# Optimization experiments

Hardware: AMD Instinct MI355X
Metric: run time of the kernel (lower is better)

## Reference

```python
import jax, jax.numpy as jnp
import numpy as np

DIM = 1280
NUM_HEADS = 16
HEAD_DIM = DIM // NUM_HEADS  # 80
SEQ = 3072


def rotate_half(x):
    half = x.shape[-1] // 2
    return jnp.concatenate([-x[..., half:], x[..., :half]], axis=-1)


def apply_rotary_pos_emb_vision(t, freqs):
    # t: [seq, heads, head_dim]; freqs: [seq, head_dim//2]
    emb = jnp.concatenate([freqs, freqs], axis=-1)  # [seq, head_dim]
    cos = jnp.cos(emb)[:, None, :]
    sin = jnp.sin(emb)[:, None, :]
    return t * cos + rotate_half(t) * sin


def setup_inputs() -> dict:
    key = jax.random.key(0)
    k1, k2, k3, k4, k5 = jax.random.split(key, 5)
    hidden_states = jax.random.normal(k1, (SEQ, DIM), dtype=jnp.float32)
    rotary_pos_emb = jax.random.uniform(k2, (SEQ, HEAD_DIM // 2), dtype=jnp.float32) * 10.0
    cu_seqlens = jnp.arange(5, dtype=jnp.int32) * (SEQ // 4)  # [0,768,1536,2304,3072]
    s = 1.0 / np.sqrt(DIM)
    qkv_w = jax.random.normal(k3, (3 * DIM, DIM), dtype=jnp.float32) * s
    qkv_b = jnp.zeros((3 * DIM,), dtype=jnp.float32)
    proj_w = jax.random.normal(k4, (DIM, DIM), dtype=jnp.float32) * s
    proj_b = jnp.zeros((DIM,), dtype=jnp.float32)
    return {
        "hidden_states": hidden_states,
        "rotary_pos_emb": rotary_pos_emb,
        "cu_seqlens": cu_seqlens,
        "qkv_w": qkv_w,
        "qkv_b": qkv_b,
        "proj_w": proj_w,
        "proj_b": proj_b,
    }


def reference(hidden_states, rotary_pos_emb, cu_seqlens, qkv_w, qkv_b, proj_w, proj_b):
    seq = hidden_states.shape[0]
    qkv = hidden_states @ qkv_w.T + qkv_b  # [seq, 3*dim]
    qkv = qkv.reshape(seq, 3, NUM_HEADS, HEAD_DIM)
    q, k, v = qkv[:, 0], qkv[:, 1], qkv[:, 2]  # each [seq, heads, head_dim]

    q = apply_rotary_pos_emb_vision(q, rotary_pos_emb)
    k = apply_rotary_pos_emb_vision(k, rotary_pos_emb)

    # block-diagonal mask from cu_seqlens: tokens attend only within own segment
    pos = jnp.arange(seq)
    seg = jnp.searchsorted(cu_seqlens[1:], pos, side="right")  # segment id per token
    mask = seg[:, None] == seg[None, :]  # [seq, seq] bool

    # [heads, seq, head_dim]
    qh = q.transpose(1, 0, 2)
    kh = k.transpose(1, 0, 2)
    vh = v.transpose(1, 0, 2)

    scale = 1.0 / np.sqrt(HEAD_DIM)
    scores = jnp.einsum("hqd,hkd->hqk", qh, kh) * scale
    scores = jnp.where(mask[None], scores, jnp.finfo(scores.dtype).min)
    attn = jax.nn.softmax(scores, axis=-1)
    out = jnp.einsum("hqk,hkd->hqd", attn, vh)  # [heads, seq, head_dim]

    out = out.transpose(1, 0, 2).reshape(seq, DIM)
    return out @ proj_w.T + proj_b
```

## Files before the change

kernel.cpp:

```cpp
#include <hip/hip_runtime.h>
#include <cstdint>
#include <cstddef>

#define SEQ 3072
#define DIM 1280
#define NH 16
#define HD 80

typedef __attribute__((ext_vector_type(8))) short s16x8;
typedef __attribute__((ext_vector_type(4))) float f32x4;
typedef unsigned short u16;
typedef unsigned int u32;
typedef unsigned long long u64;

__device__ __forceinline__ u16 f2bf(float f) {
  u32 u = __builtin_bit_cast(u32, f);
  u32 r = (u + 0x7FFFu + ((u >> 16) & 1u)) >> 16;
  return (u16)r;
}
__device__ __forceinline__ float bf2f(u16 b) {
  u32 u = ((u32)b) << 16;
  return __builtin_bit_cast(float, u);
}
__device__ __forceinline__ u32 cvtpk_bf16(float lo, float hi) {
  u32 r;
  asm("v_cvt_pk_bf16_f32 %0, %1, %2" : "=v"(r) : "v"(lo), "v"(hi));
  return r;
}
__device__ __forceinline__ void gload16(const u16* g, u16* lds) {
  __builtin_amdgcn_global_load_lds((const __attribute__((address_space(1))) void*)g,
                                   (__attribute__((address_space(3))) void*)lds,
                                   16, 0, 0);
}

#define N4_A (SEQ*DIM/4)
#define N4_B (3*DIM*DIM/4)
#define N4_C (DIM*DIM/4)
#define NTAB (SEQ*(HD/2))
__global__ void cvt_kernel(const float* __restrict__ sa, u16* __restrict__ da,
                           const float* __restrict__ sb, u16* __restrict__ db,
                           const float* __restrict__ sc, u16* __restrict__ dc,
                           const float* __restrict__ freqs, float2* __restrict__ tab) {
  int i = blockIdx.x * blockDim.x + threadIdx.x;
  if (i < N4_A + N4_B + N4_C) {
    const float* s; u16* d; int j;
    if (i < N4_A)           { s = sa; d = da; j = i; }
    else if (i < N4_A+N4_B) { s = sb; d = db; j = i - N4_A; }
    else                    { s = sc; d = dc; j = i - N4_A - N4_B; }
    float4 v = ((const float4*)s)[j];
    ushort4 o;
    o.x = f2bf(v.x); o.y = f2bf(v.y); o.z = f2bf(v.z); o.w = f2bf(v.w);
    ((ushort4*)d)[j] = o;
  } else {
    int j = i - (N4_A + N4_B + N4_C);
    if (j < NTAB) {
      float f = freqs[j];
      tab[j] = make_float2(cosf(f), sinf(f));
    }
  }
}

__global__ __launch_bounds__(256)
void gemm_kernel(const u16* __restrict__ A, const u16* __restrict__ B,
                 const float* __restrict__ bias,
                 u16* __restrict__ qws, u16* __restrict__ kws, u16* __restrict__ vT,
                 int M, int N, int K)
{
  constexpr int BM = 128, BN = 128, BK = 32;
  __shared__ __align__(16) u16 As[2][BM*BK];
  __shared__ __align__(16) u16 Bs[2][BN*BK];
  const int m0 = blockIdx.y * BM, n0 = blockIdx.x * BN;
  const int tid = threadIdx.x;
  const int lane = tid & 63, wave = tid >> 6;
  const int wr = wave >> 1, wc = wave & 1;
  const int lr = lane & 15, lg = lane >> 4;

  const int c0 = tid, c1 = 256 + tid;
  const int r0 = c0 >> 2, cc0 = c0 & 3;
  const int r1 = c1 >> 2, cc1 = c1 & 3;
  const int wb0 = (tid & ~63), wb1 = 256 + (tid & ~63);

  f32x4 acc[4][4];
  #pragma unroll
  for (int i = 0; i < 4; ++i)
    #pragma unroll
    for (int j = 0; j < 4; ++j) acc[i][j] = (f32x4)0.0f;

  const int NT = K / BK;

  gload16(A + (size_t)(m0 + r0)*K + cc0*8, &As[0][0] + wb0*8);
  gload16(B + (size_t)(n0 + r0)*K + cc0*8, &Bs[0][0] + wb0*8);
  gload16(A + (size_t)(m0 + r1)*K + cc1*8, &As[0][0] + wb1*8);
  gload16(B + (size_t)(n0 + r1)*K + cc1*8, &Bs[0][0] + wb1*8);
  __syncthreads();

  int cur = 0;
  for (int t = 0; t < NT; ++t) {
    if (t + 1 < NT) {
      const int k0 = (t + 1) * BK;
      const int nxt = cur ^ 1;
      gload16(A + (size_t)(m0 + r0)*K + k0 + cc0*8, &As[nxt][0] + wb0*8);
      gload16(B + (size_t)(n0 + r0)*K + k0 + cc0*8, &Bs[nxt][0] + wb0*8);
      gload16(A + (size_t)(m0 + r1)*K + k0 + cc1*8, &As[nxt][0] + wb1*8);
      gload16(B + (size_t)(n0 + r1)*K + k0 + cc1*8, &Bs[nxt][0] + wb1*8);
    }
    s16x8 af[4], bf[4];
    #pragma unroll
    for (int i = 0; i < 4; ++i) {
      af[i] = *(const s16x8*)&As[cur][(wr*64 + i*16 + lr)*BK + lg*8];
      bf[i] = *(const s16x8*)&Bs[cur][(wc*64 + i*16 + lr)*BK + lg*8];
    }
    #pragma unroll
    for (int mi = 0; mi < 4; ++mi)
      #pragma unroll
      for (int ni = 0; ni < 4; ++ni)
        acc[mi][ni] = __builtin_amdgcn_mfma_f32_16x16x32_bf16(af[mi], bf[ni], acc[mi][ni], 0, 0, 0);
    __syncthreads();
    cur ^= 1;
  }

  #pragma unroll
  for (int ni = 0; ni < 4; ++ni) {
    const int n = n0 + wc*64 + ni*16 + lr;
    const float bv = bias[n];
    const int which = n / DIM;
    const int hd = n - which*DIM;
    const int h = hd / HD;
    const int d = hd - h*HD;
    #pragma unroll
    for (int mi = 0; mi < 4; ++mi) {
      const int mb = m0 + wr*64 + mi*16 + lg*4;
      #pragma unroll
      for (int j = 0; j < 4; ++j) {
        const u16 b = f2bf(acc[mi][ni][j] + bv);
        const int m = mb + j;
        if (which == 0)      qws[((size_t)h*SEQ + m)*HD + d] = b;
        else if (which == 1) kws[((size_t)h*SEQ + m)*HD + d] = b;
        else                 vT [((size_t)h*HD + d)*SEQ + m] = b;
      }
    }
  }
}

__global__ __launch_bounds__(128)
void gemm1_kernel(const u16* __restrict__ A, const u16* __restrict__ B,
                  const float* __restrict__ bias, float* __restrict__ fout,
                  int M, int N, int K)
{
  constexpr int BM = 128, BN = 64, BK = 32;
  __shared__ __align__(16) u16 As[2][BM*BK];
  __shared__ __align__(16) u16 Bs[2][BN*BK];
  const int m0 = blockIdx.y * BM, n0 = blockIdx.x * BN;
  const int tid = threadIdx.x;
  const int lane = tid & 63, wave = tid >> 6;
  const int lr = lane & 15, lg = lane >> 4;

  int rA[4], cA[4], wbA[4];
  #pragma unroll
  for (int i = 0; i < 4; ++i) {
    const int c = i*128 + tid;
    rA[i] = c >> 2; cA[i] = c & 3;
    wbA[i] = i*128 + (tid & ~63);
  }
  int rB[2], cB[2], wbB[2];
  #pragma unroll
  for (int i = 0; i < 2; ++i) {
    const int c = i*128 + tid;
    rB[i] = c >> 2; cB[i] = c & 3;
    wbB[i] = i*128 + (tid & ~63);
  }

  f32x4 acc[4][4];
  #pragma unroll
  for (int i = 0; i < 4; ++i)
    #pragma unroll
    for (int j = 0; j < 4; ++j) acc[i][j] = (f32x4)0.0f;

  const int NT = K / BK;

  auto stage = [&](int t, int buf) {
    const int k0 = t * BK;
    #pragma unroll
    for (int i = 0; i < 4; ++i)
      gload16(A + (size_t)(m0 + rA[i])*K + k0 + cA[i]*8, &As[buf][0] + wbA[i]*8);
    #pragma unroll
    for (int i = 0; i < 2; ++i)
      gload16(B + (size_t)(n0 + rB[i])*K + k0 + cB[i]*8, &Bs[buf][0] + wbB[i]*8);
  };

  stage(0, 0);
  __syncthreads();

  int cur = 0;
  for (int t = 0; t < NT; ++t) {
    if (t + 1 < NT) stage(t + 1, cur ^ 1);
    s16x8 af[4], bf[4];
    #pragma unroll
    for (int i = 0; i < 4; ++i) {
      af[i] = *(const s16x8*)&As[cur][(wave*64 + i*16 + lr)*BK + lg*8];
      bf[i] = *(const s16x8*)&Bs[cur][(i*16 + lr)*BK + lg*8];
    }
    #pragma unroll
    for (int mi = 0; mi < 4; ++mi)
      #pragma unroll
      for (int ni = 0; ni < 4; ++ni)
        acc[mi][ni] = __builtin_amdgcn_mfma_f32_16x16x32_bf16(af[mi], bf[ni], acc[mi][ni], 0, 0, 0);
    __syncthreads();
    cur ^= 1;
  }

  #pragma unroll
  for (int ni = 0; ni < 4; ++ni) {
    const int n = n0 + ni*16 + lr;
    const float bv = bias[n];
    #pragma unroll
    for (int mi = 0; mi < 4; ++mi) {
      const int mb = m0 + wave*64 + mi*16 + lg*4;
      #pragma unroll
      for (int j = 0; j < 4; ++j)
        fout[(size_t)(mb + j)*N + n] = acc[mi][ni][j] + bv;
    }
  }
}

__global__ void rope_apply_kernel(u16* __restrict__ q, u16* __restrict__ k,
                                  const float2* __restrict__ tab) {
  int idx = blockIdx.x*blockDim.x + threadIdx.x;
  if (idx >= NH*SEQ*5) return;
  const int c = idx % 5;
  const int s = (idx / 5) % SEQ;
  const int h = idx / (5*SEQ);
  const int d0 = c*8;
  const float2* tp = tab + s*(HD/2) + d0;
  float cs[8], sn[8];
  #pragma unroll
  for (int j = 0; j < 8; ++j) { float2 f = tp[j]; cs[j] = f.x; sn[j] = f.y; }
  const size_t base = ((size_t)h*SEQ + s)*HD;
  {
    s16x8 x = *(const s16x8*)(q + base + d0);
    s16x8 y = *(const s16x8*)(q + base + (HD/2) + d0);
    s16x8 nx, ny;
    #pragma unroll
    for (int j = 0; j < 8; ++j) {
      float xv = bf2f((u16)x[j]), yv = bf2f((u16)y[j]);
      nx[j] = (short)f2bf(xv*cs[j] - yv*sn[j]);
      ny[j] = (short)f2bf(yv*cs[j] + xv*sn[j]);
    }
    *(s16x8*)(q + base + d0) = nx;
    *(s16x8*)(q + base + (HD/2) + d0) = ny;
  }
  {
    s16x8 x = *(const s16x8*)(k + base + d0);
    s16x8 y = *(const s16x8*)(k + base + (HD/2) + d0);
    s16x8 nx, ny;
    #pragma unroll
    for (int j = 0; j < 8; ++j) {
      float xv = bf2f((u16)x[j]), yv = bf2f((u16)y[j]);
      nx[j] = (short)f2bf(xv*cs[j] - yv*sn[j]);
      ny[j] = (short)f2bf(yv*cs[j] + xv*sn[j]);
    }
    *(s16x8*)(k + base + d0) = nx;
    *(s16x8*)(k + base + (HD/2) + d0) = ny;
  }
}

struct AttnState {
  float m_run[2];
  float lp[2];
  f32x4 oacc[2][5];
};

__device__ __forceinline__ void load_kv(const u16* __restrict__ kbase,
                                        const u16* __restrict__ vbase,
                                        int lr, int lg, int kc,
                                        s16x8 (&KF)[2][3], s16x8 (&VF)[5]) {
  int kcl = kc; if (kcl > SEQ-32) kcl = SEQ-32;
  #pragma unroll
  for (int kt = 0; kt < 2; ++kt)
    #pragma unroll
    for (int s = 0; s < 3; ++s) {
      const int d0 = s*32 + lg*8;
      if (d0 < HD) KF[kt][s] = *(const s16x8*)(kbase + (size_t)(kcl + kt*16 + lr)*HD + d0);
      else         KF[kt][s] = (s16x8)(short)0;
    }
  #pragma unroll
  for (int dt = 0; dt < 5; ++dt)
    VF[dt] = *(const s16x8*)(vbase + (size_t)(dt*16 + lr)*SEQ + kcl + lg*8);
}

__device__ __forceinline__ void compute_chunk(int kc, const s16x8 (&KF)[2][3], const s16x8 (&VF)[5],
                                              const s16x8 (&qf)[2][3], AttnState& st,
                                              u16 (&P_lds)[2][16][32],
                                              int lr, int lg, int swz,
                                              int rs0, int re0, int rs1, int re1) {
  const float NEG = -__builtin_inff();
  const float DTH = 8.0f;
  const float kscale = 0.11180339887498949f * 1.44269504088896341f;

  f32x4 sacc[2][2];
  #pragma unroll
  for (int qs = 0; qs < 2; ++qs)
    #pragma unroll
    for (int kt = 0; kt < 2; ++kt) sacc[qs][kt] = (f32x4)0.0f;
  #pragma unroll
  for (int kt = 0; kt < 2; ++kt)
    #pragma unroll
    for (int s = 0; s < 3; ++s) {
      sacc[0][kt] = __builtin_amdgcn_mfma_f32_16x16x32_bf16(KF[kt][s], qf[0][s], sacc[0][kt], 0, 0, 0);
      sacc[1][kt] = __builtin_amdgcn_mfma_f32_16x16x32_bf16(KF[kt][s], qf[1][s], sacc[1][kt], 0, 0, 0);
    }

  float sv[2][8];
  #pragma unroll
  for (int qs = 0; qs < 2; ++qs)
    #pragma unroll
    for (int kt = 0; kt < 2; ++kt)
      #pragma unroll
      for (int j = 0; j < 4; ++j)
        sv[qs][kt*4+j] = sacc[qs][kt][j] * kscale;

  const bool full = __all((kc >= rs0) && (kc+32 <= re0) && (kc >= rs1) && (kc+32 <= re1));
  if (!full) {
    #pragma unroll
    for (int qs = 0; qs < 2; ++qs) {
      const int rsq = qs ? rs1 : rs0, req = qs ? re1 : re0;
      #pragma unroll
      for (int kt = 0; kt < 2; ++kt)
        #pragma unroll
        for (int j = 0; j < 4; ++j) {
          const int key = kc + kt*16 + lg*4 + j;
          if (key < rsq || key >= req) sv[qs][kt*4+j] = NEG;
        }
    }
  }

  float pc[2];
  #pragma unroll
  for (int qs = 0; qs < 2; ++qs) {
    float c = sv[qs][0];
    #pragma unroll
    for (int i = 1; i < 8; ++i) c = fmaxf(c, sv[qs][i]);
    pc[qs] = c;
  }

  const bool nore = __all((pc[0] - st.m_run[0] <= DTH) && (pc[1] - st.m_run[1] <= DTH));
  u32 pk[2][4];
  if (nore) {
    #pragma unroll
    for (int qs = 0; qs < 2; ++qs) {
      const float m = st.m_run[qs];
      float ps = 0.0f;
      #pragma unroll
      for (int i2 = 0; i2 < 4; ++i2) {
        float pa = __builtin_amdgcn_exp2f(sv[qs][2*i2]   - m);
        float pb = __builtin_amdgcn_exp2f(sv[qs][2*i2+1] - m);
        ps += pa + pb;
        pk[qs][i2] = cvtpk_bf16(pa, pb);
      }
      st.lp[qs] += ps;
    }
  } else {
    #pragma unroll
    for (int qs = 0; qs < 2; ++qs) {
      float c = pc[qs];
      c = fmaxf(c, __shfl_xor(c, 16, 64));
      c = fmaxf(c, __shfl_xor(c, 32, 64));
      const float mn = fmaxf(st.m_run[qs], c);
      const float fs = (mn == st.m_run[qs]) ? 1.0f : __builtin_amdgcn_exp2f(st.m_run[qs] - mn);
      float ps = 0.0f;
      #pragma unroll
      for (int i2 = 0; i2 < 4; ++i2) {
        float a0 = sv[qs][2*i2], a1 = sv[qs][2*i2+1];
        float pa = (a0 == NEG) ? 0.0f : __builtin_amdgcn_exp2f(a0 - mn);
        float pb = (a1 == NEG) ? 0.0f : __builtin_amdgcn_exp2f(a1 - mn);
        ps += pa + pb;
        pk[qs][i2] = cvtpk_bf16(pa, pb);
      }
      st.lp[qs] = st.lp[qs] * fs + ps;
      st.m_run[qs] = mn;
      float fr[4];
      #pragma unroll
      for (int j = 0; j < 4; ++j)
        fr[j] = __builtin_bit_cast(float,
                  __builtin_amdgcn_ds_bpermute((lg*4 + j)*4, __builtin_bit_cast(int, fs)));
      #pragma unroll
      for (int dt = 0; dt < 5; ++dt)
        #pragma unroll
        for (int j = 0; j < 4; ++j) st.oacc[qs][dt][j] *= fr[j];
    }
  }

  #pragma unroll
  for (int qs = 0; qs < 2; ++qs) {
    u64 w0 = (u64)pk[qs][0] | ((u64)pk[qs][1] << 32);
    u64 w1 = (u64)pk[qs][2] | ((u64)pk[qs][3] << 32);
    u64* P64 = (u64*)&P_lds[qs][0][0];
    P64[lr*8 + ( lg      ^ (swz<<1))] = w0;
    P64[lr*8 + ((4 + lg) ^ (swz<<1))] = w1;
  }
  s16x8 pa0 = *(const s16x8*)&P_lds[0][lr][(lg ^ swz) * 8];
  s16x8 pa1 = *(const s16x8*)&P_lds[1][lr][(lg ^ swz) * 8];

  #pragma unroll
  for (int dt = 0; dt < 5; ++dt) {
    st.oacc[0][dt] = __builtin_amdgcn_mfma_f32_16x16x32_bf16(pa0, VF[dt], st.oacc[0][dt], 0, 0, 0);
    st.oacc[1][dt] = __builtin_amdgcn_mfma_f32_16x16x32_bf16(pa1, VF[dt], st.oacc[1][dt], 0, 0, 0);
  }
}

__global__ __launch_bounds__(128)
void attn_kernel(const u16* __restrict__ qws, const u16* __restrict__ kws,
                 const u16* __restrict__ vT, const int* __restrict__ cu, int ncu,
                 u16* __restrict__ ows )
{
  __shared__ __align__(16) u16 P_lds[2][2][16][32];
  __shared__ float mstat[2][2][16];
  __shared__ float lstat[2][2][16];
  __shared__ float O_lds[32][84];
  const int h = blockIdx.x & 15;
  const int t = blockIdx.x >> 4;
  const int tid = threadIdx.x;
  const int w = tid >> 6;
  const int lane = tid & 63;
  const int lr = lane & 15, lg = lane >> 4;
  const int q0 = t*32;
  const float NEG = -__builtin_inff();

  int rs0 = cu[0], re0 = cu[1], rs1 = cu[0], re1 = cu[1];
  int ts = cu[0], te = cu[1];
  {
    const int qa = q0 + lr, qb = q0 + 16 + lr;
    for (int i = 1; i < ncu-1; ++i) {
      int lo = cu[i], hi = cu[i+1];
      if (qa    >= lo) { rs0 = lo; re0 = hi; }
      if (qb    >= lo) { rs1 = lo; re1 = hi; }
      if (q0    >= lo) { ts = lo; }
      if (q0+31 >= lo) { te = hi; }
    }
  }

  const u16* kbase = kws + (size_t)h*SEQ*HD;
  const u16* vbase = vT  + (size_t)h*HD*SEQ;

  s16x8 qf[2][3];
  #pragma unroll
  for (int qs = 0; qs < 2; ++qs)
    #pragma unroll
    for (int s = 0; s < 3; ++s) {
      int d0 = s*32 + lg*8;
      if (d0 < HD) qf[qs][s] = *(const s16x8*)(qws + ((size_t)h*SEQ + q0 + qs*16 + lr)*HD + d0);
      else         qf[qs][s] = (s16x8)(short)0;
    }

  AttnState st;
  st.m_run[0] = NEG; st.m_run[1] = NEG;
  st.lp[0] = 0.0f;   st.lp[1] = 0.0f;
  #pragma unroll
  for (int qs = 0; qs < 2; ++qs)
    #pragma unroll
    for (int dt = 0; dt < 5; ++dt) st.oacc[qs][dt] = (f32x4)0.0f;

  const int swz = (lr >> 1) & 3;

  const int kc0 = ts & ~31;
  const int nch = (te - kc0 + 31) >> 5;
  const int n_w = (nch - w + 1) >> 1;

  s16x8 kfA[2][3], vfA[5], kfB[2][3], vfB[5];
  const int kcw0 = kc0 + w*32;
  if (n_w > 0) load_kv(kbase, vbase, lr, lg, kcw0, kfA, vfA);

  int kc = kcw0, i = 0;
  for (; i + 2 <= n_w; i += 2) {
    load_kv(kbase, vbase, lr, lg, kc+64,  kfB, vfB);
    compute_chunk(kc, kfA, vfA, qf, st, P_lds[w], lr, lg, swz, rs0, re0, rs1, re1);
    load_kv(kbase, vbase, lr, lg, kc+128, kfA, vfA);
    compute_chunk(kc+64, kfB, vfB, qf, st, P_lds[w], lr, lg, swz, rs0, re0, rs1, re1);
    kc += 128;
  }
  if (i < n_w)
    compute_chunk(kc, kfA, vfA, qf, st, P_lds[w], lr, lg, swz, rs0, re0, rs1, re1);

  #pragma unroll
  for (int qs = 0; qs < 2; ++qs) {
    st.lp[qs] += __shfl_xor(st.lp[qs], 16, 64);
    st.lp[qs] += __shfl_xor(st.lp[qs], 32, 64);
  }
  if (lg == 0) {
    mstat[w][0][lr] = st.m_run[0]; lstat[w][0][lr] = st.lp[0];
    mstat[w][1][lr] = st.m_run[1]; lstat[w][1][lr] = st.lp[1];
  }
  __syncthreads();

  float fac[2][4], lin[2][4];
  #pragma unroll
  for (int qs = 0; qs < 2; ++qs)
    #pragma unroll
    for (int j = 0; j < 4; ++j) {
      const int r = lg*4 + j;
      const float m0 = mstat[0][qs][r], m1 = mstat[1][qs][r];
      const float mst = fmaxf(m0, m1);
      float lst = 0.0f;
      if (m0 != NEG) lst += lstat[0][qs][r] * __builtin_amdgcn_exp2f(m0 - mst);
      if (m1 != NEG) lst += lstat[1][qs][r] * __builtin_amdgcn_exp2f(m1 - mst);
      const float mw = w ? m1 : m0;
      fac[qs][j] = (mw == NEG) ? 0.0f : __builtin_amdgcn_exp2f(mw - mst);
      lin[qs][j] = 1.0f / lst;
    }

  if (w == 1) {
    #pragma unroll
    for (int qs = 0; qs < 2; ++qs)
      #pragma unroll
      for (int dt = 0; dt < 5; ++dt)
        #pragma unroll
        for (int j = 0; j < 4; ++j)
          O_lds[qs*16 + lg*4 + j][dt*16 + lr] = st.oacc[qs][dt][j] * fac[qs][j];
  }
  __syncthreads();
  if (w == 0) {
    #pragma unroll
    for (int qs = 0; qs < 2; ++qs)
      #pragma unroll
      for (int dt = 0; dt < 5; ++dt)
        #pragma unroll
        for (int j = 0; j < 4; ++j) {
          float v = (st.oacc[qs][dt][j] * fac[qs][j] + O_lds[qs*16 + lg*4 + j][dt*16 + lr])
                    * lin[qs][j];
          ows[(size_t)(q0 + qs*16 + lg*4 + j)*DIM + h*HD + dt*16 + lr] = f2bf(v);
        }
  }
}

extern "C" void kernel_launch(void* const* d_in, const int* in_sizes, int n_in,
                              void* d_out, int out_size, void* d_ws, size_t ws_size,
                              hipStream_t stream) {
  const float* hidden = (const float*)d_in[0];
  const float* rope   = (const float*)d_in[1];
  const int*   cu     = (const int*)d_in[2];
  const float* qkv_w  = (const float*)d_in[3];
  const float* qkv_b  = (const float*)d_in[4];
  const float* proj_w = (const float*)d_in[5];
  const float* proj_b = (const float*)d_in[6];
  float* out = (float*)d_out;
  const int ncu = in_sizes[2];

  char* ws = (char*)d_ws;
  u16* Abf = (u16*)ws; ws += (size_t)SEQ*DIM*2;
  u16* Wq  = (u16*)ws; ws += (size_t)3*DIM*DIM*2;
  u16* Wp  = (u16*)ws; ws += (size_t)DIM*DIM*2;
  u16* qws = (u16*)ws; ws += (size_t)NH*SEQ*HD*2;
  u16* kws = (u16*)ws; ws += (size_t)NH*SEQ*HD*2;
  u16* vTw = (u16*)ws; ws += (size_t)NH*SEQ*HD*2;
  u16* ows = (u16*)ws; ws += (size_t)SEQ*DIM*2;
  float2* tab = (float2*)ws; ws += (size_t)NTAB*8;

  cvt_kernel<<<(N4_A+N4_B+N4_C+NTAB+255)/256, 256, 0, stream>>>(
      hidden, Abf, qkv_w, Wq, proj_w, Wp, rope, tab);

  gemm_kernel<<<dim3(3*DIM/128, SEQ/128), 256, 0, stream>>>(
      Abf, Wq, qkv_b, qws, kws, vTw, SEQ, 3*DIM, DIM);

  rope_apply_kernel<<<(NH*SEQ*5 + 255)/256, 256, 0, stream>>>(qws, kws, tab);

  attn_kernel<<<NH*(SEQ/32), 128, 0, stream>>>(qws, kws, vTw, cu, ncu, ows);

  gemm1_kernel<<<dim3(DIM/64, SEQ/128), 128, 0, stream>>>(
      ows, Wp, proj_b, out, SEQ, DIM, DIM);
}
```

Baseline: 147.7 us.

## Double query rows per attention block and drop explicit K/V register prefetch

```diff
diff --git a/kernel.cpp b/kernel.cpp
--- a/kernel.cpp
+++ b/kernel.cpp
@@ -265,89 +265,84 @@
 }
 
 struct AttnState {
-  float m_run[2];
-  float lp[2];
-  f32x4 oacc[2][5];
+  float m_run[4];
+  float lp[4];
+  f32x4 oacc[4][5];
 };
 
-__device__ __forceinline__ void load_kv(const u16* __restrict__ kbase,
-                                        const u16* __restrict__ vbase,
-                                        int lr, int lg, int kc,
-                                        s16x8 (&KF)[2][3], s16x8 (&VF)[5]) {
-  int kcl = kc; if (kcl > SEQ-32) kcl = SEQ-32;
-  #pragma unroll
-  for (int kt = 0; kt < 2; ++kt)
-    #pragma unroll
-    for (int s = 0; s < 3; ++s) {
-      const int d0 = s*32 + lg*8;
-      if (d0 < HD) KF[kt][s] = *(const s16x8*)(kbase + (size_t)(kcl + kt*16 + lr)*HD + d0);
-      else         KF[kt][s] = (s16x8)(short)0;
-    }
-  #pragma unroll
-  for (int dt = 0; dt < 5; ++dt)
-    VF[dt] = *(const s16x8*)(vbase + (size_t)(dt*16 + lr)*SEQ + kcl + lg*8);
-}
-
-__device__ __forceinline__ void compute_chunk(int kc, const s16x8 (&KF)[2][3], const s16x8 (&VF)[5],
-                                              const s16x8 (&qf)[2][3], AttnState& st,
-                                              u16 (&P_lds)[2][16][32],
-                                              int lr, int lg, int swz,
-                                              int rs0, int re0, int rs1, int re1) {
+__device__ __forceinline__ void compute_chunk(int kc,
+    const u16* __restrict__ kbase, const u16* __restrict__ vbase,
+    const s16x8 (&qf)[4][3], AttnState& st,
+    u16 (&P_lds)[4][16][32], int lr, int lg, int swz,
+    const int (&rs)[4], const int (&re)[4]) {
   const float NEG = -__builtin_inff();
   const float DTH = 8.0f;
   const float kscale = 0.11180339887498949f * 1.44269504088896341f;
-
-  f32x4 sacc[2][2];
-  #pragma unroll
-  for (int qs = 0; qs < 2; ++qs)
+  int kcl = kc; if (kcl > SEQ-32) kcl = SEQ-32;
+
+  f32x4 sacc[4][2];
+  #pragma unroll
+  for (int qs = 0; qs < 4; ++qs)
     #pragma unroll
     for (int kt = 0; kt < 2; ++kt) sacc[qs][kt] = (f32x4)0.0f;
   #pragma unroll
-  for (int kt = 0; kt < 2; ++kt)
+  for (int kt = 0; kt < 2; ++kt) {
+    s16x8 kf[3];
     #pragma unroll
     for (int s = 0; s < 3; ++s) {
-      sacc[0][kt] = __builtin_amdgcn_mfma_f32_16x16x32_bf16(KF[kt][s], qf[0][s], sacc[0][kt], 0, 0, 0);
-      sacc[1][kt] = __builtin_amdgcn_mfma_f32_16x16x32_bf16(KF[kt][s], qf[1][s], sacc[1][kt], 0, 0, 0);
-    }
-
-  float sv[2][8];
-  #pragma unroll
-  for (int qs = 0; qs < 2; ++qs)
+      const int d0 = s*32 + lg*8;
+      if (d0 < HD) kf[s] = *(const s16x8*)(kbase + (size_t)(kcl + kt*16 + lr)*HD + d0);
+      else         kf[s] = (s16x8)(short)0;
+    }
+    #pragma unroll
+    for (int s = 0; s < 3; ++s)
+      #pragma unroll
+      for (int qs = 0; qs < 4; ++qs)
+        sacc[qs][kt] = __builtin_amdgcn_mfma_f32_16x16x32_bf16(kf[s], qf[qs][s], sacc[qs][kt], 0, 0, 0);
+  }
+
+  float sv[4][8];
+  #pragma unroll
+  for (int qs = 0; qs < 4; ++qs)
     #pragma unroll
     for (int kt = 0; kt < 2; ++kt)
       #pragma unroll
       for (int j = 0; j < 4; ++j)
         sv[qs][kt*4+j] = sacc[qs][kt][j] * kscale;
 
-  const bool full = __all((kc >= rs0) && (kc+32 <= re0) && (kc >= rs1) && (kc+32 <= re1));
-  if (!full) {
-    #pragma unroll
-    for (int qs = 0; qs < 2; ++qs) {
-      const int rsq = qs ? rs1 : rs0, req = qs ? re1 : re0;
+  bool allin = true;
+  #pragma unroll
+  for (int qs = 0; qs < 4; ++qs) allin = allin && (kc >= rs[qs]) && (kc+32 <= re[qs]);
+  if (!__all(allin)) {
+    #pragma unroll
+    for (int qs = 0; qs < 4; ++qs)
       #pragma unroll
       for (int kt = 0; kt < 2; ++kt)
         #pragma unroll
         for (int j = 0; j < 4; ++j) {
           const int key = kc + kt*16 + lg*4 + j;
-          if (key < rsq || key >= req) sv[qs][kt*4+j] = NEG;
+          if (key < rs[qs] || key >= re[qs]) sv[qs][kt*4+j] = NEG;
         }
-    }
-  }
-
-  float pc[2];
-  #pragma unroll
-  for (int qs = 0; qs < 2; ++qs) {
+  }
+
+  float pc[4];
+  #pragma unroll
+  for (int qs = 0; qs < 4; ++qs) {
     float c = sv[qs][0];
     #pragma unroll
     for (int i = 1; i < 8; ++i) c = fmaxf(c, sv[qs][i]);
     pc[qs] = c;
   }
 
-  const bool nore = __all((pc[0] - st.m_run[0] <= DTH) && (pc[1] - st.m_run[1] <= DTH));
-  u32 pk[2][4];
+  bool small = true;
+  #pragma unroll
+  for (int qs = 0; qs < 4; ++qs) small = small && (pc[qs] - st.m_run[qs] <= DTH);
+  const bool nore = __all(small);
+
+  u32 pk[4][4];
   if (nore) {
     #pragma unroll
-    for (int qs = 0; qs < 2; ++qs) {
+    for (int qs = 0; qs < 4; ++qs) {
       const float m = st.m_run[qs];
       float ps = 0.0f;
       #pragma unroll
@@ -361,7 +356,7 @@
     }
   } else {
     #pragma unroll
-    for (int qs = 0; qs < 2; ++qs) {
+    for (int qs = 0; qs < 4; ++qs) {
       float c = pc[qs];
       c = fmaxf(c, __shfl_xor(c, 16, 64));
       c = fmaxf(c, __shfl_xor(c, 32, 64));
@@ -391,20 +386,24 @@
   }
 
   #pragma unroll
-  for (int qs = 0; qs < 2; ++qs) {
+  for (int qs = 0; qs < 4; ++qs) {
     u64 w0 = (u64)pk[qs][0] | ((u64)pk[qs][1] << 32);
     u64 w1 = (u64)pk[qs][2] | ((u64)pk[qs][3] << 32);
     u64* P64 = (u64*)&P_lds[qs][0][0];
     P64[lr*8 + ( lg      ^ (swz<<1))] = w0;
     P64[lr*8 + ((4 + lg) ^ (swz<<1))] = w1;
   }
-  s16x8 pa0 = *(const s16x8*)&P_lds[0][lr][(lg ^ swz) * 8];
-  s16x8 pa1 = *(const s16x8*)&P_lds[1][lr][(lg ^ swz) * 8];
+  s16x8 pa[4];
+  #pragma unroll
+  for (int qs = 0; qs < 4; ++qs)
+    pa[qs] = *(const s16x8*)&P_lds[qs][lr][(lg ^ swz) * 8];
 
   #pragma unroll
   for (int dt = 0; dt < 5; ++dt) {
-    st.oacc[0][dt] = __builtin_amdgcn_mfma_f32_16x16x32_bf16(pa0, VF[dt], st.oacc[0][dt], 0, 0, 0);
-    st.oacc[1][dt] = __builtin_amdgcn_mfma_f32_16x16x32_bf16(pa1, VF[dt], st.oacc[1][dt], 0, 0, 0);
+    s16x8 vf = *(const s16x8*)(vbase + (size_t)(dt*16 + lr)*SEQ + kcl + lg*8);
+    #pragma unroll
+    for (int qs = 0; qs < 4; ++qs)
+      st.oacc[qs][dt] = __builtin_amdgcn_mfma_f32_16x16x32_bf16(pa[qs], vf, st.oacc[qs][dt], 0, 0, 0);
   }
 }
 
@@ -413,38 +412,42 @@
                  const u16* __restrict__ vT, const int* __restrict__ cu, int ncu,
                  u16* __restrict__ ows )
 {
-  __shared__ __align__(16) u16 P_lds[2][2][16][32];
-  __shared__ float mstat[2][2][16];
-  __shared__ float lstat[2][2][16];
-  __shared__ float O_lds[32][84];
+  __shared__ __align__(16) u16 P_lds[2][4][16][32];
+  __shared__ float mstat[2][4][16];
+  __shared__ float lstat[2][4][16];
+  __shared__ float O_lds[64][84];
   const int h = blockIdx.x & 15;
   const int t = blockIdx.x >> 4;
   const int tid = threadIdx.x;
   const int w = tid >> 6;
   const int lane = tid & 63;
   const int lr = lane & 15, lg = lane >> 4;
-  const int q0 = t*32;
+  const int q0 = t*64;
   const float NEG = -__builtin_inff();
 
-  int rs0 = cu[0], re0 = cu[1], rs1 = cu[0], re1 = cu[1];
+  int rs[4], re[4];
   int ts = cu[0], te = cu[1];
+  #pragma unroll
+  for (int qs = 0; qs < 4; ++qs) { rs[qs] = cu[0]; re[qs] = cu[1]; }
   {
-    const int qa = q0 + lr, qb = q0 + 16 + lr;
     for (int i = 1; i < ncu-1; ++i) {
       int lo = cu[i], hi = cu[i+1];
-      if (qa    >= lo) { rs0 = lo; re0 = hi; }
-      if (qb    >= lo) { rs1 = lo; re1 = hi; }
+      #pragma unroll
+      for (int qs = 0; qs < 4; ++qs) {
+        const int qa = q0 + qs*16 + lr;
+        if (qa >= lo) { rs[qs] = lo; re[qs] = hi; }
+      }
       if (q0    >= lo) { ts = lo; }
-      if (q0+31 >= lo) { te = hi; }
+      if (q0+63 >= lo) { te = hi; }
     }
   }
 
   const u16* kbase = kws + (size_t)h*SEQ*HD;
   const u16* vbase = vT  + (size_t)h*HD*SEQ;
 
-  s16x8 qf[2][3];
-  #pragma unroll
-  for (int qs = 0; qs < 2; ++qs)
+  s16x8 qf[4][3];
+  #pragma unroll
+  for (int qs = 0; qs < 4; ++qs)
     #pragma unroll
     for (int s = 0; s < 3; ++s) {
       int d0 = s*32 + lg*8;
@@ -453,48 +456,39 @@
     }
 
   AttnState st;
-  st.m_run[0] = NEG; st.m_run[1] = NEG;
-  st.lp[0] = 0.0f;   st.lp[1] = 0.0f;
-  #pragma unroll
-  for (int qs = 0; qs < 2; ++qs)
+  #pragma unroll
+  for (int qs = 0; qs < 4; ++qs) {
+    st.m_run[qs] = NEG;
+    st.lp[qs] = 0.0f;
     #pragma unroll
     for (int dt = 0; dt < 5; ++dt) st.oacc[qs][dt] = (f32x4)0.0f;
+  }
 
   const int swz = (lr >> 1) & 3;
 
   const int kc0 = ts & ~31;
   const int nch = (te - kc0 + 31) >> 5;
-  const int n_w = (nch - w + 1) >> 1;
-
-  s16x8 kfA[2][3], vfA[5], kfB[2][3], vfB[5];
-  const int kcw0 = kc0 + w*32;
-  if (n_w > 0) load_kv(kbase, vbase, lr, lg, kcw0, kfA, vfA);
-
-  int kc = kcw0, i = 0;
-  for (; i + 2 <= n_w; i += 2) {
-    load_kv(kbase, vbase, lr, lg, kc+64,  kfB, vfB);
-    compute_chunk(kc, kfA, vfA, qf, st, P_lds[w], lr, lg, swz, rs0, re0, rs1, re1);
-    load_kv(kbase, vbase, lr, lg, kc+128, kfA, vfA);
-    compute_chunk(kc+64, kfB, vfB, qf, st, P_lds[w], lr, lg, swz, rs0, re0, rs1, re1);
-    kc += 128;
-  }
-  if (i < n_w)
-    compute_chunk(kc, kfA, vfA, qf, st, P_lds[w], lr, lg, swz, rs0, re0, rs1, re1);
-
-  #pragma unroll
-  for (int qs = 0; qs < 2; ++qs) {
+
+  for (int i = w; i < nch; i += 2)
+    compute_chunk(kc0 + i*32, kbase, vbase, qf, st, P_lds[w], lr, lg, swz, rs, re);
+
+  #pragma unroll
+  for (int qs = 0; qs < 4; ++qs) {
     st.lp[qs] += __shfl_xor(st.lp[qs], 16, 64);
     st.lp[qs] += __shfl_xor(st.lp[qs], 32, 64);
   }
   if (lg == 0) {
-    mstat[w][0][lr] = st.m_run[0]; lstat[w][0][lr] = st.lp[0];
-    mstat[w][1][lr] = st.m_run[1]; lstat[w][1][lr] = st.lp[1];
+    #pragma unroll
+    for (int qs = 0; qs < 4; ++qs) {
+      mstat[w][qs][lr] = st.m_run[qs];
+      lstat[w][qs][lr] = st.lp[qs];
+    }
   }
   __syncthreads();
 
-  float fac[2][4], lin[2][4];
-  #pragma unroll
-  for (int qs = 0; qs < 2; ++qs)
+  float fac[4][4], lin[4][4];
+  #pragma unroll
+  for (int qs = 0; qs < 4; ++qs)
     #pragma unroll
     for (int j = 0; j < 4; ++j) {
       const int r = lg*4 + j;
@@ -510,7 +504,7 @@
 
   if (w == 1) {
     #pragma unroll
-    for (int qs = 0; qs < 2; ++qs)
+    for (int qs = 0; qs < 4; ++qs)
       #pragma unroll
       for (int dt = 0; dt < 5; ++dt)
         #pragma unroll
@@ -520,7 +514,7 @@
   __syncthreads();
   if (w == 0) {
     #pragma unroll
-    for (int qs = 0; qs < 2; ++qs)
+    for (int qs = 0; qs < 4; ++qs)
       #pragma unroll
       for (int dt = 0; dt < 5; ++dt)
         #pragma unroll
@@ -563,7 +557,7 @@
 
   rope_apply_kernel<<<(NH*SEQ*5 + 255)/256, 256, 0, stream>>>(qws, kws, tab);
 
-  attn_kernel<<<NH*(SEQ/32), 128, 0, stream>>>(qws, kws, vTw, cu, ncu, ows);
+  attn_kernel<<<NH*(SEQ/64), 128, 0, stream>>>(qws, kws, vTw, cu, ncu, ows);
 
   gemm1_kernel<<<dim3(DIM/64, SEQ/128), 128, 0, stream>>>(
       ows, Wp, proj_b, out, SEQ, DIM, DIM);
```

New measurement: 177.9 us. 1.2x slower.
